# Optimization experiments

Hardware: AMD Instinct MI355X
Metric: run time of the kernel (lower is better)

## Reference

```python
import jax, jax.numpy as jnp
import numpy as np

B, T, E, H, V = 64, 21, 512, 512, 10000


def _lstm_step(x, h, c, W_ih, W_hh, b):
    # PyTorch LSTMCell gate order: i, f, g, o
    gates = x @ W_ih.T + h @ W_hh.T + b  # [B, 4H]
    i, f, g, o = jnp.split(gates, 4, axis=-1)
    i, f, o = jax.nn.sigmoid(i), jax.nn.sigmoid(f), jax.nn.sigmoid(o)
    g = jnp.tanh(g)
    c_new = f * c + i * g
    h_new = o * jnp.tanh(c_new)
    return h_new, c_new


def setup_inputs() -> dict:
    key = jax.random.key(0)
    ks = jax.random.split(key, 8)
    s_ih = 1.0 / np.sqrt(H)
    return {
        "features": jax.random.normal(ks[0], (B, E), jnp.float32),
        "caption_embedding": jax.random.normal(ks[1], (B, T, E), jnp.float32),
        "W_ih": jax.random.uniform(ks[2], (4 * H, E), jnp.float32, -s_ih, s_ih),
        "W_hh": jax.random.uniform(ks[3], (4 * H, H), jnp.float32, -s_ih, s_ih),
        "b_ih": jax.random.uniform(ks[4], (4 * H,), jnp.float32, -s_ih, s_ih),
        "b_hh": jax.random.uniform(ks[5], (4 * H,), jnp.float32, -s_ih, s_ih),
        "W_lin": jax.random.uniform(ks[6], (V, H), jnp.float32, -s_ih, s_ih),
        "b_lin": jax.random.uniform(ks[7], (V,), jnp.float32, -s_ih, s_ih),
    }


def reference(features, caption_embedding, W_ih, W_hh, b_ih, b_hh, W_lin, b_lin):
    b = b_ih + b_hh
    batch = features.shape[0]
    hidden = W_hh.shape[1]
    h0 = jnp.zeros((batch, hidden), features.dtype)
    c0 = jnp.zeros((batch, hidden), features.dtype)
    # t = 0: consume image features, no output emitted
    h, c = _lstm_step(features, h0, c0, W_ih, W_hh, b)
    # t = 1..T-1: consume caption_embedding[:, t-1], emit linear(h)
    emb_seq = jnp.swapaxes(caption_embedding[:, :-1, :], 0, 1)  # [T-1, B, E]

    def body(carry, x_t):
        h, c = carry
        h, c = _lstm_step(x_t, h, c, W_ih, W_hh, b)
        out = h @ W_lin.T + b_lin  # [B, V]
        return (h, c), out

    _, outs = jax.lax.scan(body, (h, c), emb_seq)  # [T-1, B, V]
    return jnp.swapaxes(outs, 0, 1)  # [B, T-1, V]
```

## Files before the change

kernel.cpp:

```cpp
#include <hip/hip_runtime.h>
#include <hip/hip_bf16.h>


#define NB 64
#define NT 21
#define NE 512
#define NH 512
#define NV 10000
#define G4 2048
#define FLGD 16

typedef __attribute__((ext_vector_type(8))) short bf16x8;
typedef __attribute__((ext_vector_type(4))) float f32x4;
typedef __attribute__((ext_vector_type(4))) unsigned short u16x4;

#define OFF_WIH_HI   0UL
#define OFF_WIH_LO   2097152UL
#define OFF_WHH_HI   4194304UL
#define OFF_WHH_LO   6291456UL
#define OFF_WLIN_HI  8388608UL
#define OFF_XSEQ_HI  18743296UL
#define OFF_XSEQ_LO  20185088UL
#define OFF_BIAS     21626880UL
#define OFF_XIH      21635072UL
#define OFF_GHH      32645120UL
#define OFF_GHL      32776192UL
#define OFF_C        32907264UL
#define OFF_HBUF     33038336UL
#define OFF_FLG      34349056UL

__device__ inline unsigned short f2bf(float f) {
    unsigned int u = __float_as_uint(f);
    unsigned int r = u + 0x7FFFu + ((u >> 16) & 1u);
    return (unsigned short)(r >> 16);
}
__device__ inline float bf2f(unsigned short s) {
    return __uint_as_float(((unsigned int)s) << 16);
}

__device__ __forceinline__ void gl_lds16(const unsigned short* g, unsigned short* l) {
    auto gp = (const __attribute__((address_space(1))) unsigned int*)(unsigned long long)(const void*)g;
    auto lp = (__attribute__((address_space(3))) unsigned int*)(unsigned int)(unsigned long long)(void*)l;
    __builtin_amdgcn_global_load_lds(gp, lp, 16, 0, 0);
}

__device__ __forceinline__ void gl_lds16_sc(const unsigned short* g, unsigned short* l) {
    auto gp = (const __attribute__((address_space(1))) unsigned int*)(unsigned long long)(const void*)g;
    auto lp = (__attribute__((address_space(3))) unsigned int*)(unsigned int)(unsigned long long)(void*)l;
    __builtin_amdgcn_global_load_lds(gp, lp, 16, 0, 17);
}

__device__ __forceinline__ void st4_sc(unsigned int* p, unsigned int v) {
    asm volatile("global_store_dword %0, %1, off sc0 sc1" :: "v"(p), "v"(v) : "memory");
}
__device__ __forceinline__ void st8_sc(unsigned short* p, u16x4 v) {
    asm volatile("global_store_dwordx2 %0, %1, off sc0 sc1" :: "v"(p), "v"(v) : "memory");
}
__device__ __forceinline__ void st16_sc(float* p, f32x4 v) {
    asm volatile("global_store_dwordx4 %0, %1, off sc0 sc1" :: "v"(p), "v"(v) : "memory");
}

__global__ __launch_bounds__(512) void fused_all(
    const float* __restrict__ features, const float* __restrict__ cap,
    const float* __restrict__ W_ih_f, const float* __restrict__ W_hh_f,
    const float* __restrict__ b_ih, const float* __restrict__ b_hh,
    const float* __restrict__ W_lin_f, const float* __restrict__ b_lin,
    float* __restrict__ out, unsigned char* __restrict__ ws)
{
    __shared__ unsigned short Hhi[64 * 512];
    __shared__ unsigned short Hlo[64 * 512];
    __shared__ float glf[4096];
    const int tid = threadIdx.x;
    const int lane = tid & 63, wv = tid >> 6;
    const int mf = lane & 15, kg = lane >> 4;

    unsigned int* __restrict__ flg = (unsigned int*)(ws + OFF_C);
    unsigned int* __restrict__ slabctr = (unsigned int*)(ws + OFF_FLG);
    unsigned short* __restrict__ hbuf = (unsigned short*)(ws + OFF_HBUF);
    const float* __restrict__ bias = (const float*)(ws + OFF_BIAS);
    float* __restrict__ xih_base = (float*)(ws + OFF_XIH);

    if (blockIdx.x < 32) {
        const int bc = blockIdx.x;
        const int q = wv & 3;
        const int mh = wv >> 2;

        unsigned short* __restrict__ ghh = (unsigned short*)(ws + OFF_GHH);
        unsigned short* __restrict__ ghl = (unsigned short*)(ws + OFF_GHL);

        bf16x8 bh[16], blo[16];
#pragma unroll
        for (int j = 0; j < 16; ++j) {
            const float* src = W_hh_f + (size_t)(q * 512 + bc * 16 + mf) * 512 + j * 32 + kg * 8;
            float4 w0 = *(const float4*)src;
            float4 w1 = *(const float4*)(src + 4);
            float ff[8] = {w0.x, w0.y, w0.z, w0.w, w1.x, w1.y, w1.z, w1.w};
#pragma unroll
            for (int e = 0; e < 8; ++e) {
                const unsigned short h = f2bf(ff[e]);
                bh[j][e] = (short)h;
                blo[j][e] = (short)f2bf(ff[e] - bf2f(h));
            }
        }

        const int crow = tid >> 3;
        const int cp = tid & 7;
        const int c0 = bc * 16 + cp * 2;
        const int jch = bc * 2 + (cp >> 2);
        const int sw = (jch * 64 + crow) * 8 + ((cp * 2) & 7);
        float creg0 = 0.f, creg1 = 0.f;

        float2 xp[4];
        auto load_xp = [&](int tt) {
            const float* __restrict__ xq = xih_base + (size_t)tt * NB * G4;
#pragma unroll
            for (int g2 = 0; g2 < 4; ++g2)
                xp[g2] = *(const float2*)&xq[crow * G4 + g2 * 512 + c0];
        };

        if (tid == 0) {
            while (__hip_atomic_load(&slabctr[0], __ATOMIC_RELAXED, __HIP_MEMORY_SCOPE_AGENT) < 16u)
                __builtin_amdgcn_s_sleep(1);
        }
        __syncthreads();
        load_xp(0);

        for (int t = 0; t < NT; ++t) {
            f32x4 acc[2];
            acc[0] = (f32x4){0.f, 0.f, 0.f, 0.f};
            acc[1] = (f32x4){0.f, 0.f, 0.f, 0.f};

            if (t > 0) {
                const int rd = (t + 1) & 1;
                const unsigned short* __restrict__ ghh_r = ghh + rd * (NB * NH);
                const unsigned short* __restrict__ ghl_r = ghl + rd * (NB * NH);

                if (lane < 4) {
                    const unsigned int* fp = flg + ((size_t)(t - 1) * 32 + wv * 4 + lane) * FLGD;
                    while (__hip_atomic_load(fp, __ATOMIC_RELAXED, __HIP_MEMORY_SCOPE_AGENT) == 0u)
                        __builtin_amdgcn_s_sleep(1);
                } else if (lane == 4) {
                    const unsigned int* sp = slabctr + (size_t)t * FLGD;
                    while (__hip_atomic_load(sp, __ATOMIC_RELAXED, __HIP_MEMORY_SCOPE_AGENT) < 16u)
                        __builtin_amdgcn_s_sleep(1);
                }
#pragma unroll
                for (int pp = 0; pp < 4; ++pp) {
                    const int jj = (wv * 4 + pp) * 2;
                    gl_lds16_sc(ghh_r + (jj    ) * 512 + lane * 8, &Hhi[(jj    ) * 512 + lane * 8]);
                    gl_lds16_sc(ghh_r + (jj + 1) * 512 + lane * 8, &Hhi[(jj + 1) * 512 + lane * 8]);
                }
#pragma unroll
                for (int pp = 0; pp < 4; ++pp) {
                    const int jj = (wv * 4 + pp) * 2;
                    gl_lds16_sc(ghl_r + (jj    ) * 512 + lane * 8, &Hlo[(jj    ) * 512 + lane * 8]);
                    gl_lds16_sc(ghl_r + (jj + 1) * 512 + lane * 8, &Hlo[(jj + 1) * 512 + lane * 8]);
                }
                asm volatile("s_waitcnt vmcnt(8)" ::: "memory");
                __builtin_amdgcn_s_barrier();
                load_xp(t);
#pragma unroll
                for (int kt = 0; kt < 16; ++kt) {
                    const int j = kt * 4 + kg;
#pragma unroll
                    for (int m = 0; m < 2; ++m) {
                        const int row = mh * 32 + m * 16 + mf;
                        bf16x8 a_hi = *(const bf16x8*)&Hhi[(j * 64 + row) * 8];
                        acc[m] = __builtin_amdgcn_mfma_f32_16x16x32_bf16(a_hi, bh[kt], acc[m], 0, 0, 0);
                        acc[m] = __builtin_amdgcn_mfma_f32_16x16x32_bf16(a_hi, blo[kt], acc[m], 0, 0, 0);
                    }
                }
                asm volatile("s_waitcnt vmcnt(0)" ::: "memory");
                __builtin_amdgcn_s_barrier();
#pragma unroll
                for (int kt = 0; kt < 16; ++kt) {
                    const int j = kt * 4 + kg;
#pragma unroll
                    for (int m = 0; m < 2; ++m) {
                        const int row = mh * 32 + m * 16 + mf;
                        bf16x8 a_lo = *(const bf16x8*)&Hlo[(j * 64 + row) * 8];
                        acc[m] = __builtin_amdgcn_mfma_f32_16x16x32_bf16(a_lo, bh[kt], acc[m], 0, 0, 0);
                    }
                }
            }

#pragma unroll
            for (int m = 0; m < 2; ++m) {
                const int row = mh * 32 + m * 16 + kg * 4;
#pragma unroll
                for (int r = 0; r < 4; ++r)
                    glf[(q * 64 + row + r) * 16 + mf] = acc[m][r];
            }
            __syncthreads();

            {
                unsigned short* __restrict__ ghh_w = ghh + (t & 1) * (NB * NH);
                unsigned short* __restrict__ ghl_w = ghl + (t & 1) * (NB * NH);
                const float2 g0 = *(const float2*)&glf[(0 * 64 + crow) * 16 + cp * 2];
                const float2 g1 = *(const float2*)&glf[(1 * 64 + crow) * 16 + cp * 2];
                const float2 g2 = *(const float2*)&glf[(2 * 64 + crow) * 16 + cp * 2];
                const float2 g3 = *(const float2*)&glf[(3 * 64 + crow) * 16 + cp * 2];
                const float gi0 = g0.x + xp[0].x, gi1 = g0.y + xp[0].y;
                const float gf0 = g1.x + xp[1].x, gf1 = g1.y + xp[1].y;
                const float gg0 = g2.x + xp[2].x, gg1 = g2.y + xp[2].y;
                const float go0 = g3.x + xp[3].x, go1 = g3.y + xp[3].y;
                const float i0 = 1.f / (1.f + __expf(-gi0)), i1 = 1.f / (1.f + __expf(-gi1));
                const float f0 = 1.f / (1.f + __expf(-gf0)), f1 = 1.f / (1.f + __expf(-gf1));
                const float ga0 = tanhf(gg0),                ga1 = tanhf(gg1);
                const float o0 = 1.f / (1.f + __expf(-go0)), o1 = 1.f / (1.f + __expf(-go1));
                const float cn0 = f0 * creg0 + i0 * ga0;
                const float cn1 = f1 * creg1 + i1 * ga1;
                creg0 = cn0; creg1 = cn1;
                const float h0 = o0 * tanhf(cn0);
                const float h1 = o1 * tanhf(cn1);
                const unsigned short hi0 = f2bf(h0), hi1 = f2bf(h1);
                const unsigned short lo0 = f2bf(h0 - bf2f(hi0)), lo1 = f2bf(h1 - bf2f(hi1));
                const unsigned int hpack = (unsigned int)hi0 | ((unsigned int)hi1 << 16);
                const unsigned int lpack = (unsigned int)lo0 | ((unsigned int)lo1 << 16);
                st4_sc((unsigned int*)&ghh_w[sw], hpack);
                st4_sc((unsigned int*)&ghl_w[sw], lpack);
                if (t >= 1)
                    st4_sc((unsigned int*)&hbuf[(size_t)(t - 1) * (NB * NH) + crow * NH + c0], hpack);
            }

            asm volatile("s_waitcnt vmcnt(0)" ::: "memory");
            __syncthreads();
            if (tid == 0) {
                unsigned int one = 1u;
                unsigned int* fp = flg + ((size_t)t * 32 + bc) * FLGD;
                asm volatile("global_store_dword %0, %1, off sc0 sc1" :: "v"(fp), "v"(one) : "memory");
            }
        }
        asm volatile("s_waitcnt vmcnt(0)" ::: "memory");
        return;
    }

    const int g = blockIdx.x - 32;
    const int mw2 = (wv >> 2) * 32, nw2 = (wv & 3) * 32;

    {
        unsigned short* wih_hi = (unsigned short*)(ws + OFF_WIH_HI);
        unsigned short* wih_lo = (unsigned short*)(ws + OFF_WIH_LO);
        unsigned short* xs_hi = (unsigned short*)(ws + OFF_XSEQ_HI);
        unsigned short* xs_lo = (unsigned short*)(ws + OFF_XSEQ_LO);
        float* bias_w = (float*)(ws + OFF_BIAS);
        int idx = g * 512 + tid;
        for (int it = 0; it < 4; ++it, idx += 114688) {
            if (idx < 262144) {
                const int i4 = idx * 4;
                float4 w = *(const float4*)(W_ih_f + i4);
                u16x4 hi, lo;
                hi.x = f2bf(w.x); lo.x = f2bf(w.x - bf2f(hi.x));
                hi.y = f2bf(w.y); lo.y = f2bf(w.y - bf2f(hi.y));
                hi.z = f2bf(w.z); lo.z = f2bf(w.z - bf2f(hi.z));
                hi.w = f2bf(w.w); lo.w = f2bf(w.w - bf2f(hi.w));
                st8_sc(wih_hi + i4, hi);
                st8_sc(wih_lo + i4, lo);
            } else if (idx < 434176) {
                const int i4 = (idx - 262144) * 4;
                const int e = i4 & 511;
                const int b = (i4 >> 9) & 63;
                const int t2 = i4 >> 15;
                float4 x = (t2 == 0) ? *(const float4*)(features + b * NE + e)
                                     : *(const float4*)(cap + b * (NT * NE) + (t2 - 1) * NE + e);
                u16x4 hi, lo;
                hi.x = f2bf(x.x); lo.x = f2bf(x.x - bf2f(hi.x));
                hi.y = f2bf(x.y); lo.y = f2bf(x.y - bf2f(hi.y));
                hi.z = f2bf(x.z); lo.z = f2bf(x.z - bf2f(hi.z));
                hi.w = f2bf(x.w); lo.w = f2bf(x.w - bf2f(hi.w));
                st8_sc(xs_hi + i4, hi);
                st8_sc(xs_lo + i4, lo);
            } else if (idx < 434688) {
                const int j = (idx - 434176) * 4;
                float4 a = *(const float4*)(b_ih + j);
                float4 b = *(const float4*)(b_hh + j);
                f32x4 s;
                s[0] = a.x + b.x; s[1] = a.y + b.y; s[2] = a.z + b.z; s[3] = a.w + b.w;
                st16_sc(bias_w + j, s);
            }
        }
        asm volatile("s_waitcnt vmcnt(0)" ::: "memory");
        __syncthreads();
        if (tid == 0) {
            __hip_atomic_fetch_add(&slabctr[24 * FLGD], 1u, __ATOMIC_RELAXED, __HIP_MEMORY_SCOPE_AGENT);
            while (__hip_atomic_load(&slabctr[24 * FLGD], __ATOMIC_RELAXED, __HIP_MEMORY_SCOPE_AGENT) < 224u)
                __builtin_amdgcn_s_sleep(1);
        }
        __syncthreads();
    }

    {
        const unsigned short* __restrict__ xh = (const unsigned short*)(ws + OFF_XSEQ_HI);
        const unsigned short* __restrict__ xl = (const unsigned short*)(ws + OFF_XSEQ_LO);
        const unsigned short* __restrict__ wih_h = (const unsigned short*)(ws + OFF_WIH_HI);
        const unsigned short* __restrict__ wih_l = (const unsigned short*)(ws + OFF_WIH_LO);

        unsigned short* Ah2 = Hhi;
        unsigned short* Al2 = Hhi + 4096;
        unsigned short* Bh2 = Hhi + 8192;
        unsigned short* Bl2 = Hhi + 16384;

        const int ntile = (g < 112) ? 2 : 1;
        for (int p = 0; p < ntile; ++p) {
            const int T = (p == 0) ? g : 224 + g;
            const int slab = T >> 4, ct = T & 15;
            const unsigned short* __restrict__ xhA = xh + (size_t)slab * 64 * 512;
            const unsigned short* __restrict__ xlA = xl + (size_t)slab * 64 * 512;

            auto stageA = [&](int buf, int k0) {
                if (tid < 256) {
                    const int s = tid, r = s >> 2, kc = (s & 3) * 8;
                    gl_lds16(xhA + (size_t)r * 512 + k0 + kc, &Ah2[buf * 2048 + s * 8]);
                    gl_lds16(xlA + (size_t)r * 512 + k0 + kc, &Al2[buf * 2048 + s * 8]);
                } else {
#pragma unroll
                    for (int h2 = 0; h2 < 2; ++h2) {
                        const int s = h2 * 256 + (tid - 256), r = s >> 2, kc = (s & 3) * 8;
                        gl_lds16(wih_h + (size_t)(ct * 128 + r) * 512 + k0 + kc, &Bh2[buf * 4096 + s * 8]);
                        gl_lds16(wih_l + (size_t)(ct * 128 + r) * 512 + k0 + kc, &Bl2[buf * 4096 + s * 8]);
                    }
                }
            };

            f32x4 acc2[2][2];
#pragma unroll
            for (int i = 0; i < 2; i++)
#pragma unroll
                for (int j = 0; j < 2; j++) acc2[i][j] = (f32x4){0.f, 0.f, 0.f, 0.f};

            stageA(0, 0);
            for (int kt = 0; kt < 16; ++kt) {
                __syncthreads();
                const int cur = kt & 1;
                if (kt < 15) stageA(cur ^ 1, (kt + 1) * 32);
                bf16x8 ah_[2], al_[2], bh_[2], bl_[2];
#pragma unroll
                for (int i = 0; i < 2; i++) {
                    ah_[i] = *(const bf16x8*)&Ah2[cur * 2048 + (mw2 + i * 16 + mf) * 32 + kg * 8];
                    al_[i] = *(const bf16x8*)&Al2[cur * 2048 + (mw2 + i * 16 + mf) * 32 + kg * 8];
                    bh_[i] = *(const bf16x8*)&Bh2[cur * 4096 + (nw2 + i * 16 + mf) * 32 + kg * 8];
                    bl_[i] = *(const bf16x8*)&Bl2[cur * 4096 + (nw2 + i * 16 + mf) * 32 + kg * 8];
                }
#pragma unroll
                for (int i = 0; i < 2; i++)
#pragma unroll
                    for (int j = 0; j < 2; j++) {
                        acc2[i][j] = __builtin_amdgcn_mfma_f32_16x16x32_bf16(ah_[i], bh_[j], acc2[i][j], 0, 0, 0);
                        acc2[i][j] = __builtin_amdgcn_mfma_f32_16x16x32_bf16(ah_[i], bl_[j], acc2[i][j], 0, 0, 0);
                        acc2[i][j] = __builtin_amdgcn_mfma_f32_16x16x32_bf16(al_[i], bh_[j], acc2[i][j], 0, 0, 0);
                    }
            }
#pragma unroll
            for (int i = 0; i < 2; i++)
#pragma unroll
                for (int j = 0; j < 2; j++) {
                    const int col = ct * 128 + nw2 + j * 16 + mf;
                    const float bb = bias[col];
#pragma unroll
                    for (int r = 0; r < 4; r++) {
                        const int row = slab * 64 + mw2 + i * 16 + kg * 4 + r;
                        st4_sc((unsigned int*)&xih_base[(size_t)row * G4 + col],
                               __float_as_uint(acc2[i][j][r] + bb));
                    }
                }
            asm volatile("s_waitcnt vmcnt(0)" ::: "memory");
            __syncthreads();
            if (tid == 0)
                __hip_atomic_fetch_add(&slabctr[slab * FLGD], 1u, __ATOMIC_RELAXED, __HIP_MEMORY_SCOPE_AGENT);
            __syncthreads();
        }
    }

    {
        unsigned short* wlin_w = (unsigned short*)(ws + OFF_WLIN_HI);
        int idx = g * 512 + tid;
        for (int it = 0; it < 12; ++it, idx += 114688) {
            if (idx < 1280000) {
                const int i4 = idx * 4;
                float4 w = *(const float4*)(W_lin_f + i4);
                u16x4 hi;
                hi.x = f2bf(w.x); hi.y = f2bf(w.y); hi.z = f2bf(w.z); hi.w = f2bf(w.w);
                st8_sc(wlin_w + i4, hi);
            }
        }
        asm volatile("s_waitcnt vmcnt(0)" ::: "memory");
        __syncthreads();
        if (tid == 0) {
            __hip_atomic_fetch_add(&slabctr[25 * FLGD], 1u, __ATOMIC_RELAXED, __HIP_MEMORY_SCOPE_AGENT);
            while (__hip_atomic_load(&slabctr[25 * FLGD], __ATOMIC_RELAXED, __HIP_MEMORY_SCOPE_AGENT) < 224u)
                __builtin_amdgcn_s_sleep(1);
        }
        __syncthreads();
    }

    const unsigned short* __restrict__ wlin = (const unsigned short*)(ws + OFF_WLIN_HI);
    const int jt = g % 79;
    const int rshare = g / 79;
    const int nshare = (jt < 66) ? 3 : 2;
    const int n0g = jt * 128;

    unsigned short* __restrict__ AsB = Hhi;
    unsigned short* __restrict__ BsB = Hhi + 4096;

    for (int tt = rshare; tt < NT - 1; tt += nshare) {
        if (wv == 0) {
            const unsigned int* fp = flg + ((size_t)(tt + 1) * 32 + (lane & 31)) * FLGD;
            while (__hip_atomic_load(fp, __ATOMIC_RELAXED, __HIP_MEMORY_SCOPE_AGENT) == 0u)
                __builtin_amdgcn_s_sleep(2);
        }
        __syncthreads();

        const unsigned short* __restrict__ hbA = hbuf + (size_t)tt * (NB * NH);
        auto stageC = [&](int buf, int k0) {
            if (tid < 256) {
                const int s = tid;
                const int r = s >> 2, kcol = (s & 3) * 8;
                gl_lds16_sc(hbA + (size_t)r * 512 + k0 + kcol, &AsB[buf * 2048 + s * 8]);
            } else {
#pragma unroll
                for (int h2 = 0; h2 < 2; ++h2) {
                    const int s = h2 * 256 + (tid - 256);
                    const int r = s >> 2, kcol = (s & 3) * 8;
                    gl_lds16(wlin + (size_t)(n0g + r) * 512 + k0 + kcol, &BsB[buf * 4096 + s * 8]);
                }
            }
        };

        f32x4 acc2[2][2];
#pragma unroll
        for (int i = 0; i < 2; i++)
#pragma unroll
            for (int j = 0; j < 2; j++) acc2[i][j] = (f32x4){0.f, 0.f, 0.f, 0.f};

        stageC(0, 0);
        for (int kt = 0; kt < 16; ++kt) {
            __syncthreads();
            const int cur = kt & 1;
            if (kt < 15) stageC(cur ^ 1, (kt + 1) * 32);
            bf16x8 af[2], bfv[2];
#pragma unroll
            for (int i = 0; i < 2; i++) {
                af[i]  = *(const bf16x8*)&AsB[cur * 2048 + (mw2 + i * 16 + mf) * 32 + kg * 8];
                bfv[i] = *(const bf16x8*)&BsB[cur * 4096 + (nw2 + i * 16 + mf) * 32 + kg * 8];
            }
#pragma unroll
            for (int i = 0; i < 2; i++)
#pragma unroll
                for (int j = 0; j < 2; j++)
                    acc2[i][j] = __builtin_amdgcn_mfma_f32_16x16x32_bf16(af[i], bfv[j], acc2[i][j], 0, 0, 0);
        }
#pragma unroll
        for (int i = 0; i < 2; i++)
#pragma unroll
            for (int j = 0; j < 2; j++) {
                const int col = n0g + nw2 + j * 16 + mf;
                if (col < NV) {
                    const float bl = b_lin[col];
#pragma unroll
                    for (int r = 0; r < 4; r++) {
                        const int b_ = mw2 + i * 16 + kg * 4 + r;
                        out[(size_t)b_ * ((NT - 1) * NV) + (size_t)tt * NV + col] = acc2[i][j][r] + bl;
                    }
                }
            }
        __syncthreads();
    }
}

extern "C" void kernel_launch(void* const* d_in, const int* in_sizes, int n_in,
                              void* d_out, int out_size, void* d_ws, size_t ws_size,
                              hipStream_t stream)
{
    const float* features = (const float*)d_in[0];
    const float* cap      = (const float*)d_in[1];
    const float* W_ih     = (const float*)d_in[2];
    const float* W_hh     = (const float*)d_in[3];
    const float* b_ih     = (const float*)d_in[4];
    const float* b_hh     = (const float*)d_in[5];
    const float* W_lin    = (const float*)d_in[6];
    const float* b_lin    = (const float*)d_in[7];
    float* out = (float*)d_out;
    unsigned char* ws = (unsigned char*)d_ws;

    (void)hipMemsetAsync(ws + OFF_C, 0, (size_t)NT * 32 * FLGD * sizeof(unsigned int), stream);
    (void)hipMemsetAsync(ws + OFF_FLG, 0, (size_t)32 * FLGD * sizeof(unsigned int), stream);

    hipLaunchKernelGGL(fused_all, dim3(256), dim3(512), 0, stream,
                       features, cap, W_ih, W_hh, b_ih, b_hh, W_lin, b_lin, out, ws);
}
```

Measured before the change: 262.6 us.

## Split recurrent step flag into hi/lo halves to overlap h exchange

The per-step completion flag becomes two flags: one raised after the hi-part bf16 h stores and one after the lo-part and output stores. Consumers wait on the hi flag, issue the hi loads, then wait on the lo flag before loading the lo part, so transfer of the next state overlaps the producer's remaining stores. Spin waits are merged into a single wave-level __any loop, and the two memsets are combined into one. This adds a second flag array and an extra barrier per step, and relies on the ordering between the sc0/sc1 stores and the flag stores.

```diff
diff --git a/kernel.cpp b/kernel.cpp
--- a/kernel.cpp
+++ b/kernel.cpp
@@ -16,8 +16,6 @@
 
 #define OFF_WIH_HI   0UL
 #define OFF_WIH_LO   2097152UL
-#define OFF_WHH_HI   4194304UL
-#define OFF_WHH_LO   6291456UL
 #define OFF_WLIN_HI  8388608UL
 #define OFF_XSEQ_HI  18743296UL
 #define OFF_XSEQ_LO  20185088UL
@@ -26,8 +24,9 @@
 #define OFF_GHH      32645120UL
 #define OFF_GHL      32776192UL
 #define OFF_C        32907264UL
+#define OFF_CB       32950272UL
+#define OFF_SLB      32993280UL
 #define OFF_HBUF     33038336UL
-#define OFF_FLG      34349056UL
 
 __device__ inline unsigned short f2bf(float f) {
     unsigned int u = __float_as_uint(f);
@@ -74,8 +73,9 @@
     const int lane = tid & 63, wv = tid >> 6;
     const int mf = lane & 15, kg = lane >> 4;
 
-    unsigned int* __restrict__ flg = (unsigned int*)(ws + OFF_C);
-    unsigned int* __restrict__ slabctr = (unsigned int*)(ws + OFF_FLG);
+    unsigned int* __restrict__ flgA = (unsigned int*)(ws + OFF_C);
+    unsigned int* __restrict__ flgB = (unsigned int*)(ws + OFF_CB);
+    unsigned int* __restrict__ slb  = (unsigned int*)(ws + OFF_SLB);
     unsigned short* __restrict__ hbuf = (unsigned short*)(ws + OFF_HBUF);
     const float* __restrict__ bias = (const float*)(ws + OFF_BIAS);
     float* __restrict__ xih_base = (float*)(ws + OFF_XIH);
@@ -119,7 +119,7 @@
         };
 
         if (tid == 0) {
-            while (__hip_atomic_load(&slabctr[0], __ATOMIC_RELAXED, __HIP_MEMORY_SCOPE_AGENT) < 16u)
+            while (__hip_atomic_load(&slb[0], __ATOMIC_RELAXED, __HIP_MEMORY_SCOPE_AGENT) < 16u)
                 __builtin_amdgcn_s_sleep(1);
         }
         __syncthreads();
@@ -135,28 +135,36 @@
                 const unsigned short* __restrict__ ghh_r = ghh + rd * (NB * NH);
                 const unsigned short* __restrict__ ghl_r = ghl + rd * (NB * NH);
 
-                if (lane < 4) {
-                    const unsigned int* fp = flg + ((size_t)(t - 1) * 32 + wv * 4 + lane) * FLGD;
-                    while (__hip_atomic_load(fp, __ATOMIC_RELAXED, __HIP_MEMORY_SCOPE_AGENT) == 0u)
+                {
+                    const unsigned int* p = flgA + ((size_t)(t - 1) * 32 + bc) * FLGD;
+                    unsigned int tgt = 0u;
+                    if (lane < 4)       { p = flgA + ((size_t)(t - 1) * 32 + wv * 4 + lane) * FLGD; tgt = 1u; }
+                    else if (lane == 4) { p = slb + (size_t)t * FLGD; tgt = 16u; }
+                    while (__any(__hip_atomic_load(p, __ATOMIC_RELAXED, __HIP_MEMORY_SCOPE_AGENT) < tgt))
                         __builtin_amdgcn_s_sleep(1);
-                } else if (lane == 4) {
-                    const unsigned int* sp = slabctr + (size_t)t * FLGD;
-                    while (__hip_atomic_load(sp, __ATOMIC_RELAXED, __HIP_MEMORY_SCOPE_AGENT) < 16u)
-                        __builtin_amdgcn_s_sleep(1);
-                }
+                }
+                __builtin_amdgcn_sched_barrier(0);
 #pragma unroll
                 for (int pp = 0; pp < 4; ++pp) {
                     const int jj = (wv * 4 + pp) * 2;
                     gl_lds16_sc(ghh_r + (jj    ) * 512 + lane * 8, &Hhi[(jj    ) * 512 + lane * 8]);
                     gl_lds16_sc(ghh_r + (jj + 1) * 512 + lane * 8, &Hhi[(jj + 1) * 512 + lane * 8]);
                 }
+                __builtin_amdgcn_sched_barrier(0);
+                {
+                    const unsigned int* p = flgB + ((size_t)(t - 1) * 32 + bc) * FLGD;
+                    unsigned int tgt = 0u;
+                    if (lane < 4) { p = flgB + ((size_t)(t - 1) * 32 + wv * 4 + lane) * FLGD; tgt = 1u; }
+                    while (__any(__hip_atomic_load(p, __ATOMIC_RELAXED, __HIP_MEMORY_SCOPE_AGENT) < tgt))
+                        __builtin_amdgcn_s_sleep(1);
+                }
+                __builtin_amdgcn_sched_barrier(0);
 #pragma unroll
                 for (int pp = 0; pp < 4; ++pp) {
                     const int jj = (wv * 4 + pp) * 2;
                     gl_lds16_sc(ghl_r + (jj    ) * 512 + lane * 8, &Hlo[(jj    ) * 512 + lane * 8]);
                     gl_lds16_sc(ghl_r + (jj + 1) * 512 + lane * 8, &Hlo[(jj + 1) * 512 + lane * 8]);
                 }
-                asm volatile("s_waitcnt vmcnt(8)" ::: "memory");
                 __builtin_amdgcn_s_barrier();
                 load_xp(t);
 #pragma unroll
@@ -219,17 +227,16 @@
                 const unsigned int lpack = (unsigned int)lo0 | ((unsigned int)lo1 << 16);
                 st4_sc((unsigned int*)&ghh_w[sw], hpack);
                 st4_sc((unsigned int*)&ghl_w[sw], lpack);
-                if (t >= 1)
-                    st4_sc((unsigned int*)&hbuf[(size_t)(t - 1) * (NB * NH) + crow * NH + c0], hpack);
-            }
-
+                const int sl = (t == 0) ? 0 : t - 1;
+                st4_sc((unsigned int*)&hbuf[(size_t)sl * (NB * NH) + crow * NH + c0], hpack);
+            }
+
+            asm volatile("s_waitcnt vmcnt(2)" ::: "memory");
+            __builtin_amdgcn_s_barrier();
+            if (tid == 0) st4_sc(flgA + ((size_t)t * 32 + bc) * FLGD, 1u);
             asm volatile("s_waitcnt vmcnt(0)" ::: "memory");
-            __syncthreads();
-            if (tid == 0) {
-                unsigned int one = 1u;
-                unsigned int* fp = flg + ((size_t)t * 32 + bc) * FLGD;
-                asm volatile("global_store_dword %0, %1, off sc0 sc1" :: "v"(fp), "v"(one) : "memory");
-            }
+            __builtin_amdgcn_s_barrier();
+            if (tid == 0) st4_sc(flgB + ((size_t)t * 32 + bc) * FLGD, 1u);
         }
         asm volatile("s_waitcnt vmcnt(0)" ::: "memory");
         return;
@@ -282,8 +289,8 @@
         asm volatile("s_waitcnt vmcnt(0)" ::: "memory");
         __syncthreads();
         if (tid == 0) {
-            __hip_atomic_fetch_add(&slabctr[24 * FLGD], 1u, __ATOMIC_RELAXED, __HIP_MEMORY_SCOPE_AGENT);
-            while (__hip_atomic_load(&slabctr[24 * FLGD], __ATOMIC_RELAXED, __HIP_MEMORY_SCOPE_AGENT) < 224u)
+            __hip_atomic_fetch_add(&slb[24 * FLGD], 1u, __ATOMIC_RELAXED, __HIP_MEMORY_SCOPE_AGENT);
+            while (__hip_atomic_load(&slb[24 * FLGD], __ATOMIC_RELAXED, __HIP_MEMORY_SCOPE_AGENT) < 224u)
                 __builtin_amdgcn_s_sleep(1);
         }
         __syncthreads();
@@ -366,7 +373,7 @@
             asm volatile("s_waitcnt vmcnt(0)" ::: "memory");
             __syncthreads();
             if (tid == 0)
-                __hip_atomic_fetch_add(&slabctr[slab * FLGD], 1u, __ATOMIC_RELAXED, __HIP_MEMORY_SCOPE_AGENT);
+                __hip_atomic_fetch_add(&slb[slab * FLGD], 1u, __ATOMIC_RELAXED, __HIP_MEMORY_SCOPE_AGENT);
             __syncthreads();
         }
     }
@@ -386,8 +393,8 @@
         asm volatile("s_waitcnt vmcnt(0)" ::: "memory");
         __syncthreads();
         if (tid == 0) {
-            __hip_atomic_fetch_add(&slabctr[25 * FLGD], 1u, __ATOMIC_RELAXED, __HIP_MEMORY_SCOPE_AGENT);
-            while (__hip_atomic_load(&slabctr[25 * FLGD], __ATOMIC_RELAXED, __HIP_MEMORY_SCOPE_AGENT) < 224u)
+            __hip_atomic_fetch_add(&slb[25 * FLGD], 1u, __ATOMIC_RELAXED, __HIP_MEMORY_SCOPE_AGENT);
+            while (__hip_atomic_load(&slb[25 * FLGD], __ATOMIC_RELAXED, __HIP_MEMORY_SCOPE_AGENT) < 224u)
                 __builtin_amdgcn_s_sleep(1);
         }
         __syncthreads();
@@ -404,7 +411,7 @@
 
     for (int tt = rshare; tt < NT - 1; tt += nshare) {
         if (wv == 0) {
-            const unsigned int* fp = flg + ((size_t)(tt + 1) * 32 + (lane & 31)) * FLGD;
+            const unsigned int* fp = flgB + ((size_t)(tt + 1) * 32 + (lane & 31)) * FLGD;
             while (__hip_atomic_load(fp, __ATOMIC_RELAXED, __HIP_MEMORY_SCOPE_AGENT) == 0u)
                 __builtin_amdgcn_s_sleep(2);
         }
@@ -482,8 +489,7 @@
     float* out = (float*)d_out;
     unsigned char* ws = (unsigned char*)d_ws;
 
-    (void)hipMemsetAsync(ws + OFF_C, 0, (size_t)NT * 32 * FLGD * sizeof(unsigned int), stream);
-    (void)hipMemsetAsync(ws + OFF_FLG, 0, (size_t)32 * FLGD * sizeof(unsigned int), stream);
+    (void)hipMemsetAsync(ws + OFF_C, 0, 87680, stream);
 
     hipLaunchKernelGGL(fused_all, dim3(256), dim3(512), 0, stream,
                        features, cap, W_ih, W_hh, b_ih, b_hh, W_lin, b_lin, out, ws);
```

Result: no change. 259.9 us (-1.0%).
